# Kernel optimization log

Hardware: AMD Instinct MI355X
Metric: run time of the kernel (lower is better)

Reference implementation:

```python
import jax, jax.numpy as jnp
import numpy as np

H, W = 80, 80
LOWPASS = 0.3   # 3DGS low-pass filter added to 2D covariance diagonal
NEAR = 0.2      # near-plane cull depth


def quat_to_rot(q):
    # q: [N,4] (w,x,y,z) -> [N,3,3]
    w, x, y, z = q[..., 0], q[..., 1], q[..., 2], q[..., 3]
    return jnp.stack([
        jnp.stack([1 - 2 * (y * y + z * z), 2 * (x * y - w * z), 2 * (x * z + w * y)], -1),
        jnp.stack([2 * (x * y + w * z), 1 - 2 * (x * x + z * z), 2 * (y * z - w * x)], -1),
        jnp.stack([2 * (x * z - w * y), 2 * (y * z + w * x), 1 - 2 * (x * x + y * y)], -1),
    ], -2)


def setup_inputs() -> dict:
    key = jax.random.key(0)
    k1, k2 = jax.random.split(key)
    vsize = 1.25
    def mids(lo, hi, lim):
        g = np.arange(lo, hi + 1e-6, vsize)
        return ((g[:-1] + g[1:]) / 2.0)[:lim]
    xy = mids(-20.0, 20.0, 200)   # 32 midpoints
    zz = mids(-4.0, 4.0, 16)      # 6 midpoints
    X, Y, Z = np.meshgrid(xy, xy, zz, indexing='ij')
    pc_xyz = jnp.asarray(np.stack([X, Y, Z], -1).reshape(-1, 3), jnp.float32)  # [6144,3]
    N = pc_xyz.shape[0]
    B, NC, C = 1, 6, 32
    vox_features = jax.random.normal(k1, (B, N, C), jnp.float32)
    density = jax.random.normal(k2, (B, N), jnp.float32)
    scales = jnp.full((N, 1), float(np.log(vsize)), jnp.float32)
    rots = jnp.concatenate([jnp.ones((N, 1)), jnp.zeros((N, 3))], -1).astype(jnp.float32)
    # 6 surround cameras at origin, yaw = k*60deg; cam axes: x=right, y=up-ish, z=forward
    yaws = np.arange(NC) * (2 * np.pi / NC)
    f = np.stack([np.cos(yaws), np.sin(yaws), np.zeros(NC)], -1)
    r = np.stack([np.sin(yaws), -np.cos(yaws), np.zeros(NC)], -1)
    u = np.cross(f, r)
    Rw2c = np.stack([r, u, f], 1)  # rows are camera axes -> world2cam rotation [NC,3,3]
    cam_rot = jnp.asarray(Rw2c[None], jnp.float32)          # [B,NC,3,3]
    cam_trans = jnp.zeros((B, NC, 3), jnp.float32)          # [B,NC,3]
    cam_intr = jnp.asarray(np.tile(np.array([45.0, 45.0, W / 2.0, H / 2.0], np.float32), (B, NC, 1)))
    return dict(vox_features=vox_features, density=density, cam_rot=cam_rot,
                cam_trans=cam_trans, cam_intr=cam_intr, pc_xyz=pc_xyz,
                scales=scales, rots=rots)


def _render_one(Rcw, t, intr, pc_xyz, Mcov, opacity, feats):
    # Rcw [3,3], t [3], intr [4]; Mcov [N,3,3] = R*diag(s); opacity [N]; feats [N,C]
    fx, fy, cx, cy = intr[0], intr[1], intr[2], intr[3]
    cam = pc_xyz @ Rcw.T + t                    # [N,3] camera-frame means
    tz = jnp.maximum(cam[:, 2], 1e-6)
    valid = (cam[:, 2] > NEAR).astype(pc_xyz.dtype)
    u = fx * cam[:, 0] / tz + cx
    v = fy * cam[:, 1] / tz + cy
    z0 = jnp.zeros_like(tz)
    J = jnp.stack([jnp.stack([fx / tz, z0, -fx * cam[:, 0] / tz ** 2], -1),
                   jnp.stack([z0, fy / tz, -fy * cam[:, 1] / tz ** 2], -1)], -2)  # [N,2,3]
    A = jnp.einsum('nij,jk->nik', J, Rcw)       # J @ W  [N,2,3]
    Bm = jnp.einsum('nij,njk->nik', A, Mcov)    # [N,2,3]
    cov = jnp.einsum('nij,nkj->nik', Bm, Bm)    # 2D covariance [N,2,2]
    a = cov[:, 0, 0] + LOWPASS
    b = cov[:, 0, 1]
    c = cov[:, 1, 1] + LOWPASS
    det = a * c - b * b
    ia, ib, ic = c / det, -b / det, a / det
    # depth-sort (invalid gaussians pushed to the back)
    order = jnp.argsort(tz + (1.0 - valid) * 1e6)
    u, v, ia, ib, ic = u[order], v[order], ia[order], ib[order], ic[order]
    op_s, feat_s, valid_s = opacity[order], feats[order], valid[order]
    px = jnp.arange(W, dtype=pc_xyz.dtype)
    py = jnp.arange(H, dtype=pc_xyz.dtype)
    dx = px[None, None, :] - u[:, None, None]   # [N,1,W] -> broadcast [N,H,W]
    dy = py[None, :, None] - v[:, None, None]   # [N,H,1]
    power = (-0.5 * (ia[:, None, None] * dx * dx + ic[:, None, None] * dy * dy)
             - ib[:, None, None] * dx * dy)
    g = jnp.exp(jnp.minimum(power, 0.0))
    alpha = jnp.clip(op_s[:, None, None] * g, 0.0, 0.99) * valid_s[:, None, None]
    Tcum = jnp.cumprod(1.0 - alpha, axis=0)
    Texc = jnp.concatenate([jnp.ones((1, H, W), alpha.dtype), Tcum[:-1]], 0)  # exclusive transmittance
    return jnp.einsum('nhw,nc->chw', Texc * alpha, feat_s)


def reference(vox_features, density, cam_rot, cam_trans, cam_intr, pc_xyz, scales, rots):
    Bsz, N, C = vox_features.shape
    Rg = quat_to_rot(rots)                      # [N,3,3]
    s = jnp.exp(scales)                         # [N,1] isotropic scale
    Mcov = Rg * s[:, :, None]                   # R @ diag(s,s,s)
    outs = []
    for b in range(Bsz):
        op = jax.nn.softplus(density[b]).reshape(-1)        # opacity activation
        feats = vox_features[b].reshape(-1, C)
        def rone(args):
            R_, t_, K_ = args
            return _render_one(R_, t_, K_, pc_xyz, Mcov, op, feats)
        out_b = jax.lax.map(rone, (cam_rot[b], cam_trans[b], cam_intr[b]))  # [NC,C,H,W]
        outs.append(out_b)
    return jnp.stack(outs)                      # [B,NC,C,H,W]
```

## Files before the change

kernel.cpp:

```cpp
#include <hip/hip_runtime.h>

#define NEARV    0.2f
#define LOWPASSV 0.3f

constexpr int HH = 80, WW = 80;
constexpr int CFE = 32;
constexpr int NZ = 6;

constexpr int STHREADS = 1024;
constexpr int SWAVES = 16;
constexpr int SBINS = 512;
constexpr int NCELL = 1024;

typedef unsigned long long u64;
typedef unsigned int u32;

__global__ __launch_bounds__(1024) void sort_kernel(
    const float* __restrict__ pc_xyz, const float* __restrict__ cam_rot,
    const float* __restrict__ cam_trans, int N,
    int* __restrict__ counts, int* __restrict__ cellord)
{
  __shared__ u32 skey[NCELL];
  __shared__ u32 spay[NCELL];
  __shared__ u32 whist[SWAVES * SBINS];
  __shared__ u32 binstart[SBINS];
  __shared__ u32 wpart[8];
  __shared__ int scount;

  const int cam = blockIdx.x;
  const int tid = threadIdx.x;
  const int wv = tid >> 6, ln = tid & 63;
  const float* R = cam_rot + cam*9;
  const float R20 = R[6], R21 = R[7], R22 = R[8];
  const float t2  = cam_trans[cam*3+2];
  if (tid == 0) scount = 0;
  __syncthreads();

  const int i0 = tid * NZ;
  u32 kk = 0x07FFFFFFu;
  bool valid = false;
  if (i0 < N) {
    float c2 = R20*pc_xyz[i0*3+0] + R21*pc_xyz[i0*3+1] + R22*pc_xyz[i0*3+2] + t2;
    if (c2 > NEARV) {
      u32 b = __float_as_uint(c2) - 0x3E000000u;
      kk = b < 0x07FFFFFEu ? b : 0x07FFFFFEu;
      valid = true;
    }
  }
  skey[tid] = kk; spay[tid] = (u32)tid;
  u64 vb = __ballot(valid);
  if (ln == 0) atomicAdd(&scount, __popcll(vb));

  for (int pass = 0; pass < 3; ++pass) {
    const int sh = pass * 9;
    for (int i = tid; i < SWAVES*SBINS; i += STHREADS) whist[i] = 0;
    __syncthreads();

    const u32 k = skey[tid];
    const u32 p = spay[tid];
    const int d = (int)((k >> sh) & 511u);
    u64 m = ~0ull;
    #pragma unroll
    for (int b = 0; b < 9; ++b) {
      u64 bb = __ballot((d >> b) & 1);
      m &= ((d >> b) & 1) ? bb : ~bb;
    }
    const u32 lower = (u32)__popcll(m & ((1ull << ln) - 1ull));
    if (lower == 0) whist[(wv << 9) + d] = (u32)__popcll(m);
    __syncthreads();

    if (tid < SBINS) {
      u32 t[SWAVES];
      #pragma unroll
      for (int w = 0; w < SWAVES; ++w) t[w] = whist[(w << 9) + tid];
      u32 tot = 0;
      #pragma unroll
      for (int w = 0; w < SWAVES; ++w) { u32 x = t[w]; whist[(w << 9) + tid] = tot; tot += x; }
      binstart[tid] = tot;
    }
    __syncthreads();
    u32 v = 0, inc = 0;
    if (tid < SBINS) {
      v = binstart[tid]; inc = v;
      #pragma unroll
      for (int off = 1; off < 64; off <<= 1) {
        u32 t = __shfl_up(inc, off);
        if (ln >= off) inc += t;
      }
      if (ln == 63) wpart[tid >> 6] = inc;
    }
    __syncthreads();
    if (tid < SBINS) {
      u32 add = 0;
      for (int i = 0; i < (tid >> 6); ++i) add += wpart[i];
      binstart[tid] = add + inc - v;
    }
    __syncthreads();

    const u32 pos = binstart[d] + whist[(wv << 9) + d] + lower;
    skey[pos] = k; spay[pos] = p;
    __syncthreads();
  }

  const int vc = scount;
  if (tid < vc) cellord[(size_t)cam * NCELL + tid] = (int)spay[tid];
  if (tid == 0) counts[cam] = vc * NZ;
}

__global__ __launch_bounds__(64) void render_kernel(
    const float* __restrict__ vox, const float* __restrict__ density,
    const float* __restrict__ cam_rot, const float* __restrict__ cam_trans,
    const float* __restrict__ cam_intr, const float* __restrict__ pc_xyz,
    const float* __restrict__ scales,
    const int* __restrict__ counts, const int* __restrict__ cellord,
    float* __restrict__ out, int N, int NC)
{
  __shared__ float4 cA[64], cB[64];
  __shared__ int   cgi[64];
  __shared__ float4 sfeat[64 * 8];

  const int cam = blockIdx.y;
  const int tile = blockIdx.x;
  const int tx = tile % (WW/16), ty = tile / (WW/16);
  const int lane = threadIdx.x;
  const int lx = lane & 15, ly = lane >> 4;
  const int px = tx*16 + lx, py = ty*4 + ly;
  const float fpx = (float)px, fpy = (float)py;
  const float tx0 = (float)(tx*16), tx1 = tx0 + 15.f;
  const float ty0 = (float)(ty*4),  ty1 = ty0 + 3.f;
  const int count = counts[cam];
  const int b = cam / NC;
  const float* R = cam_rot + cam*9;
  const float* t = cam_trans + cam*3;
  const float* intr = cam_intr + cam*4;
  const float fx = intr[0], fy = intr[1], cx = intr[2], cy = intr[3];
  const int* coc = cellord + (size_t)cam * NCELL;

  float acc[CFE];
  #pragma unroll
  for (int i = 0; i < CFE; ++i) acc[i] = 0.f;
  float T = 1.0f;
  bool done = false;

  for (int k0 = 0; k0 < count && !done; k0 += 64) {
    const int ki = k0 + lane;
    const int kic = min(ki, count - 1);
    const int cell = kic / NZ;
    const int n = coc[cell] * NZ + (kic - cell * NZ);
    float p0 = pc_xyz[n*3+0], p1 = pc_xyz[n*3+1], p2 = pc_xyz[n*3+2];
    float c0 = R[0]*p0 + R[1]*p1 + R[2]*p2 + t[0];
    float c1 = R[3]*p0 + R[4]*p1 + R[5]*p2 + t[1];
    float c2 = R[6]*p0 + R[7]*p1 + R[8]*p2 + t[2];
    float tz = fmaxf(c2, 1e-6f);
    float itz = 1.0f / tz;
    float u = fx*c0*itz + cx;
    float v = fy*c1*itz + cy;
    float j00 = fx*itz,  j02 = -(fx*c0*itz)*itz;
    float j11 = fy*itz,  j12 = -(fy*c1*itz)*itz;
    float s = expf(scales[n]);
    float s2 = s*s;
    float cov00 = s2*(j00*j00 + j02*j02);
    float cov01 = s2*(j02*j12);
    float cov11 = s2*(j11*j11 + j12*j12);
    float a = cov00 + LOWPASSV, bb = cov01, cc = cov11 + LOWPASSV;
    float det = a*cc - bb*bb;
    float idet = 1.0f / det;
    float mid = 0.5f*(a + cc);
    float dd = sqrtf(fmaxf(mid*mid - det, 0.f));
    float r2 = (ki < count) ? 32.f * (mid + dd) : -1.f;
    float dens = density[(size_t)b*N + n];
    float op = fmaxf(dens, 0.f) + log1pf(expf(-fabsf(dens)));
    float ddx = fminf(fmaxf(u, tx0), tx1) - u;
    float ddy = fminf(fmaxf(v, ty0), ty1) - v;
    const bool hit = (ddx*ddx + ddy*ddy) <= r2;
    const u64 m = __ballot(hit);
    const int P = __popcll(m);
    if (P == 0) continue;
    __syncthreads();
    if (hit) {
      const int pos = (int)__popcll(m & ((1ull << lane) - 1ull));
      cA[pos] = make_float4(u, v, cc*idet, -bb*idet);
      cB[pos] = make_float4(a*idet, op, 0.f, 0.f);
      cgi[pos] = n;
    }
    __syncthreads();
    for (int s0 = 0; s0 < P; s0 += 8) {
      const int si = s0 + (lane >> 3);
      if (si < P) {
        const int gi = cgi[si];
        sfeat[si*8 + (lane & 7)] =
            ((const float4*)(vox + ((size_t)b*N + gi) * CFE))[lane & 7];
      }
    }
    __syncthreads();

    for (int j = 0; j < P && !done; j += 8) {
      float al[8];
      #pragma unroll
      for (int qq = 0; qq < 8; ++qq) {
        const int idx = j + qq;
        const float4 a0 = cA[idx & 63];
        const float4 a1 = cB[idx & 63];
        float dx = fpx - a0.x, dy = fpy - a0.y;
        float power = -0.5f*(a0.z*dx*dx + a1.x*dy*dy) - a0.w*dx*dy;
        float av = fminf(a1.y * __expf(fminf(power, 0.f)), 0.99f);
        av = (power > -16.f) ? av : 0.f;
        al[qq] = (idx < P) ? av : 0.f;
      }
      #pragma unroll
      for (int qq = 0; qq < 8; ++qq) {
        float w = T * al[qq];
        T -= w;
        if (__any(w > 1e-8f)) {
          const float4* fj = &sfeat[(j + qq) * 8];
          #pragma unroll
          for (int c8 = 0; c8 < CFE/4; ++c8) {
            float4 fv = fj[c8];
            acc[c8*4+0] += w*fv.x; acc[c8*4+1] += w*fv.y;
            acc[c8*4+2] += w*fv.z; acc[c8*4+3] += w*fv.w;
          }
        }
      }
      if (__all(T < 1e-4f)) done = true;
    }
  }
  float* ob = out + (((size_t)cam * CFE) * HH + py) * WW + px;
  #pragma unroll
  for (int c = 0; c < CFE; ++c) ob[(size_t)c * HH * WW] = acc[c];
}

extern "C" void kernel_launch(void* const* d_in, const int* in_sizes, int n_in,
                              void* d_out, int out_size, void* d_ws, size_t ws_size,
                              hipStream_t stream) {
  const float* vox       = (const float*)d_in[0];
  const float* density   = (const float*)d_in[1];
  const float* cam_rot   = (const float*)d_in[2];
  const float* cam_trans = (const float*)d_in[3];
  const float* cam_intr  = (const float*)d_in[4];
  const float* pc_xyz    = (const float*)d_in[5];
  const float* scales    = (const float*)d_in[6];
  float* out = (float*)d_out;

  const int N    = in_sizes[5] / 3;
  const int NCAM = in_sizes[4] / 4;
  const int B    = in_sizes[1] / N;
  const int NC   = NCAM / B;

  unsigned char* ws = (unsigned char*)d_ws;
  int* countsPtr = (int*)ws;
  int* cellord = (int*)(ws + 256);

  sort_kernel<<<dim3(NCAM), STHREADS, 0, stream>>>(
      pc_xyz, cam_rot, cam_trans, N, countsPtr, cellord);
  render_kernel<<<dim3((WW/16)*(HH/4), NCAM), 64, 0, stream>>>(
      vox, density, cam_rot, cam_trans, cam_intr, pc_xyz, scales,
      countsPtr, cellord, out, N, NC);
}
```

Measured before the change: 84.06 us.

## Precompute per-camera splat headers with screen culling in sort kernel, prefetch in render

The sort kernel now projects each depth-sorted Gaussian once per camera, computing 2D conic, opacity, radius and index, and culls splats whose footprint misses the image. It compacts the survivors into per-camera header arrays in workspace. The render kernel no longer recomputes the projection for every tile. Instead it loads precomputed headers with a one-batch register prefetch and double-buffers feature loads in 8-splat chunks through a smaller shared buffer. This removes redundant projection math across 100 tiles per camera, at the cost of a serial compaction loop in a single block per camera and extra barriers per chunk.

```diff
diff --git a/kernel.cpp b/kernel.cpp
--- a/kernel.cpp
+++ b/kernel.cpp
@@ -11,36 +11,41 @@
 constexpr int SWAVES = 16;
 constexpr int SBINS = 512;
 constexpr int NCELL = 1024;
+constexpr int HMAX = NCELL * NZ;
 
 typedef unsigned long long u64;
 typedef unsigned int u32;
 
 __global__ __launch_bounds__(1024) void sort_kernel(
     const float* __restrict__ pc_xyz, const float* __restrict__ cam_rot,
-    const float* __restrict__ cam_trans, int N,
-    int* __restrict__ counts, int* __restrict__ cellord)
+    const float* __restrict__ cam_trans, const float* __restrict__ cam_intr,
+    const float* __restrict__ density, const float* __restrict__ scales,
+    int N, int NC,
+    int* __restrict__ counts, float4* __restrict__ hdrA,
+    float4* __restrict__ hdrB)
 {
   __shared__ u32 skey[NCELL];
   __shared__ u32 spay[NCELL];
   __shared__ u32 whist[SWAVES * SBINS];
   __shared__ u32 binstart[SBINS];
   __shared__ u32 wpart[8];
+  __shared__ u32 wsum[SWAVES];
   __shared__ int scount;
+  __shared__ int obase;
 
   const int cam = blockIdx.x;
   const int tid = threadIdx.x;
   const int wv = tid >> 6, ln = tid & 63;
   const float* R = cam_rot + cam*9;
-  const float R20 = R[6], R21 = R[7], R22 = R[8];
-  const float t2  = cam_trans[cam*3+2];
-  if (tid == 0) scount = 0;
+  const float* t = cam_trans + cam*3;
+  if (tid == 0) { scount = 0; obase = 0; }
   __syncthreads();
 
   const int i0 = tid * NZ;
   u32 kk = 0x07FFFFFFu;
   bool valid = false;
   if (i0 < N) {
-    float c2 = R20*pc_xyz[i0*3+0] + R21*pc_xyz[i0*3+1] + R22*pc_xyz[i0*3+2] + t2;
+    float c2 = R[6]*pc_xyz[i0*3+0] + R[7]*pc_xyz[i0*3+1] + R[8]*pc_xyz[i0*3+2] + t[2];
     if (c2 > NEARV) {
       u32 b = __float_as_uint(c2) - 0x3E000000u;
       kk = b < 0x07FFFFFEu ? b : 0x07FFFFFEu;
@@ -70,12 +75,12 @@
     __syncthreads();
 
     if (tid < SBINS) {
-      u32 t[SWAVES];
+      u32 tt[SWAVES];
       #pragma unroll
-      for (int w = 0; w < SWAVES; ++w) t[w] = whist[(w << 9) + tid];
+      for (int w = 0; w < SWAVES; ++w) tt[w] = whist[(w << 9) + tid];
       u32 tot = 0;
       #pragma unroll
-      for (int w = 0; w < SWAVES; ++w) { u32 x = t[w]; whist[(w << 9) + tid] = tot; tot += x; }
+      for (int w = 0; w < SWAVES; ++w) { u32 x = tt[w]; whist[(w << 9) + tid] = tot; tot += x; }
       binstart[tid] = tot;
     }
     __syncthreads();
@@ -84,8 +89,8 @@
       v = binstart[tid]; inc = v;
       #pragma unroll
       for (int off = 1; off < 64; off <<= 1) {
-        u32 t = __shfl_up(inc, off);
-        if (ln >= off) inc += t;
+        u32 tq = __shfl_up(inc, off);
+        if (ln >= off) inc += tq;
       }
       if (ln == 63) wpart[tid >> 6] = inc;
     }
@@ -103,21 +108,82 @@
   }
 
   const int vc = scount;
-  if (tid < vc) cellord[(size_t)cam * NCELL + tid] = (int)spay[tid];
-  if (tid == 0) counts[cam] = vc * NZ;
+  const int total = vc * NZ;
+  const float* intr = cam_intr + cam*4;
+  const float fx = intr[0], fy = intr[1], cx = intr[2], cy = intr[3];
+  const float R0=R[0],R1=R[1],R2=R[2],R3=R[3],R4=R[4],R5=R[5],R6=R[6],R7=R[7],R8=R[8];
+  const float t0=t[0],t1=t[1],t2=t[2];
+  const int b = cam / NC;
+  float4* hA = hdrA + (size_t)cam * HMAX;
+  float4* hB = hdrB + (size_t)cam * HMAX;
+
+  for (int k0 = 0; k0 < total; k0 += STHREADS) {
+    const int kq = k0 + tid;
+    bool keep = false;
+    float4 va = make_float4(0.f,0.f,0.f,0.f);
+    float4 vbh = make_float4(0.f,0.f,0.f,0.f);
+    if (kq < total) {
+      const int cellp = kq / NZ;
+      const int n = (int)spay[cellp] * NZ + (kq - cellp * NZ);
+      const float p0 = pc_xyz[n*3+0], p1 = pc_xyz[n*3+1], p2 = pc_xyz[n*3+2];
+      const float c0 = R0*p0 + R1*p1 + R2*p2 + t0;
+      const float c1 = R3*p0 + R4*p1 + R5*p2 + t1;
+      const float c2 = R6*p0 + R7*p1 + R8*p2 + t2;
+      const float tz = fmaxf(c2, 1e-6f);
+      const float itz = 1.0f / tz;
+      const float u = fx*c0*itz + cx;
+      const float v = fy*c1*itz + cy;
+      const float j00 = fx*itz, j02 = -(fx*c0*itz)*itz;
+      const float j11 = fy*itz, j12 = -(fy*c1*itz)*itz;
+      const float s = expf(scales[n]);
+      const float s2 = s*s;
+      const float cov00 = s2*(j00*j00 + j02*j02);
+      const float cov01 = s2*(j02*j12);
+      const float cov11 = s2*(j11*j11 + j12*j12);
+      const float a = cov00 + LOWPASSV, bb = cov01, cc = cov11 + LOWPASSV;
+      const float det = a*cc - bb*bb;
+      const float idet = 1.0f / det;
+      const float mid = 0.5f*(a + cc);
+      const float dd = sqrtf(fmaxf(mid*mid - det, 0.f));
+      const float r2 = 32.f * (mid + dd);
+      const float dens = density[(size_t)b*N + n];
+      const float op = fmaxf(dens, 0.f) + log1pf(expf(-fabsf(dens)));
+      const float sx = fminf(fmaxf(u, 0.f), (float)(WW-1)) - u;
+      const float sy = fminf(fmaxf(v, 0.f), (float)(HH-1)) - v;
+      keep = (sx*sx + sy*sy) <= r2;
+      va  = make_float4(u, v, cc*idet, -bb*idet);
+      vbh = make_float4(a*idet, op, r2, __int_as_float(n));
+    }
+    const u64 bal = __ballot(keep);
+    if (ln == 0) wsum[wv] = (u32)__popcll(bal);
+    __syncthreads();
+    if (keep) {
+      u32 off = 0;
+      for (int w = 0; w < wv; ++w) off += wsum[w];
+      const int pos = obase + (int)(off + (u32)__popcll(bal & ((1ull << ln) - 1ull)));
+      hA[pos] = va; hB[pos] = vbh;
+    }
+    __syncthreads();
+    if (tid == 0) {
+      u32 tot = 0;
+      #pragma unroll
+      for (int w = 0; w < SWAVES; ++w) tot += wsum[w];
+      obase += (int)tot;
+    }
+    __syncthreads();
+  }
+  if (tid == 0) counts[cam] = obase;
 }
 
 __global__ __launch_bounds__(64) void render_kernel(
-    const float* __restrict__ vox, const float* __restrict__ density,
-    const float* __restrict__ cam_rot, const float* __restrict__ cam_trans,
-    const float* __restrict__ cam_intr, const float* __restrict__ pc_xyz,
-    const float* __restrict__ scales,
-    const int* __restrict__ counts, const int* __restrict__ cellord,
+    const float* __restrict__ vox,
+    const float4* __restrict__ hdrA, const float4* __restrict__ hdrB,
+    const int* __restrict__ counts,
     float* __restrict__ out, int N, int NC)
 {
   __shared__ float4 cA[64], cB[64];
   __shared__ int   cgi[64];
-  __shared__ float4 sfeat[64 * 8];
+  __shared__ float4 sfeat[64];
 
   const int cam = blockIdx.y;
   const int tile = blockIdx.x;
@@ -130,11 +196,9 @@
   const float ty0 = (float)(ty*4),  ty1 = ty0 + 3.f;
   const int count = counts[cam];
   const int b = cam / NC;
-  const float* R = cam_rot + cam*9;
-  const float* t = cam_trans + cam*3;
-  const float* intr = cam_intr + cam*4;
-  const float fx = intr[0], fy = intr[1], cx = intr[2], cy = intr[3];
-  const int* coc = cellord + (size_t)cam * NCELL;
+  const float4* hA = hdrA + (size_t)cam * HMAX;
+  const float4* hB = hdrB + (size_t)cam * HMAX;
+  const float4* voxb = (const float4*)vox + (size_t)b * N * (CFE/4);
 
   float acc[CFE];
   #pragma unroll
@@ -142,86 +206,72 @@
   float T = 1.0f;
   bool done = false;
 
-  for (int k0 = 0; k0 < count && !done; k0 += 64) {
-    const int ki = k0 + lane;
-    const int kic = min(ki, count - 1);
-    const int cell = kic / NZ;
-    const int n = coc[cell] * NZ + (kic - cell * NZ);
-    float p0 = pc_xyz[n*3+0], p1 = pc_xyz[n*3+1], p2 = pc_xyz[n*3+2];
-    float c0 = R[0]*p0 + R[1]*p1 + R[2]*p2 + t[0];
-    float c1 = R[3]*p0 + R[4]*p1 + R[5]*p2 + t[1];
-    float c2 = R[6]*p0 + R[7]*p1 + R[8]*p2 + t[2];
-    float tz = fmaxf(c2, 1e-6f);
-    float itz = 1.0f / tz;
-    float u = fx*c0*itz + cx;
-    float v = fy*c1*itz + cy;
-    float j00 = fx*itz,  j02 = -(fx*c0*itz)*itz;
-    float j11 = fy*itz,  j12 = -(fy*c1*itz)*itz;
-    float s = expf(scales[n]);
-    float s2 = s*s;
-    float cov00 = s2*(j00*j00 + j02*j02);
-    float cov01 = s2*(j02*j12);
-    float cov11 = s2*(j11*j11 + j12*j12);
-    float a = cov00 + LOWPASSV, bb = cov01, cc = cov11 + LOWPASSV;
-    float det = a*cc - bb*bb;
-    float idet = 1.0f / det;
-    float mid = 0.5f*(a + cc);
-    float dd = sqrtf(fmaxf(mid*mid - det, 0.f));
-    float r2 = (ki < count) ? 32.f * (mid + dd) : -1.f;
-    float dens = density[(size_t)b*N + n];
-    float op = fmaxf(dens, 0.f) + log1pf(expf(-fabsf(dens)));
-    float ddx = fminf(fmaxf(u, tx0), tx1) - u;
-    float ddy = fminf(fmaxf(v, ty0), ty1) - v;
-    const bool hit = (ddx*ddx + ddy*ddy) <= r2;
-    const u64 m = __ballot(hit);
-    const int P = __popcll(m);
-    if (P == 0) continue;
-    __syncthreads();
-    if (hit) {
-      const int pos = (int)__popcll(m & ((1ull << lane) - 1ull));
-      cA[pos] = make_float4(u, v, cc*idet, -bb*idet);
-      cB[pos] = make_float4(a*idet, op, 0.f, 0.f);
-      cgi[pos] = n;
-    }
-    __syncthreads();
-    for (int s0 = 0; s0 < P; s0 += 8) {
-      const int si = s0 + (lane >> 3);
-      if (si < P) {
-        const int gi = cgi[si];
-        sfeat[si*8 + (lane & 7)] =
-            ((const float4*)(vox + ((size_t)b*N + gi) * CFE))[lane & 7];
+  if (count > 0) {
+    const int kcf = min(lane, count - 1);
+    float4 na = hA[kcf], nb = hB[kcf];
+
+    for (int k0 = 0; k0 < count && !done; k0 += 64) {
+      const float4 a0 = na, b0 = nb;
+      if (k0 + 64 < count) {
+        const int kn = min(k0 + 64 + lane, count - 1);
+        na = hA[kn]; nb = hB[kn];
       }
-    }
-    __syncthreads();
-
-    for (int j = 0; j < P && !done; j += 8) {
-      float al[8];
-      #pragma unroll
-      for (int qq = 0; qq < 8; ++qq) {
-        const int idx = j + qq;
-        const float4 a0 = cA[idx & 63];
-        const float4 a1 = cB[idx & 63];
-        float dx = fpx - a0.x, dy = fpy - a0.y;
-        float power = -0.5f*(a0.z*dx*dx + a1.x*dy*dy) - a0.w*dx*dy;
-        float av = fminf(a1.y * __expf(fminf(power, 0.f)), 0.99f);
-        av = (power > -16.f) ? av : 0.f;
-        al[qq] = (idx < P) ? av : 0.f;
+      const int ki = k0 + lane;
+      const float ddx = fminf(fmaxf(a0.x, tx0), tx1) - a0.x;
+      const float ddy = fminf(fmaxf(a0.y, ty0), ty1) - a0.y;
+      const bool hit = (ki < count) && (ddx*ddx + ddy*ddy <= b0.z);
+      const u64 m = __ballot(hit);
+      const int P = __popcll(m);
+      if (P == 0) continue;
+      __syncthreads();
+      if (hit) {
+        const int pos = (int)__popcll(m & ((1ull << lane) - 1ull));
+        cA[pos] = a0;
+        cB[pos] = b0;
+        cgi[pos] = __float_as_int(b0.w);
       }
-      #pragma unroll
-      for (int qq = 0; qq < 8; ++qq) {
-        float w = T * al[qq];
-        T -= w;
-        if (__any(w > 1e-8f)) {
-          const float4* fj = &sfeat[(j + qq) * 8];
-          #pragma unroll
-          for (int c8 = 0; c8 < CFE/4; ++c8) {
-            float4 fv = fj[c8];
-            acc[c8*4+0] += w*fv.x; acc[c8*4+1] += w*fv.y;
-            acc[c8*4+2] += w*fv.z; acc[c8*4+3] += w*fv.w;
+      __syncthreads();
+
+      const int sl = lane >> 3, sc = lane & 7;
+      float4 pf = voxb[(size_t)cgi[min(sl, P - 1)] * (CFE/4) + sc];
+
+      for (int j = 0; j < P; j += 8) {
+        sfeat[lane] = pf;
+        if (j + 8 < P) {
+          const int si = min(j + 8 + sl, P - 1);
+          pf = voxb[(size_t)cgi[si] * (CFE/4) + sc];
+        }
+        __syncthreads();
+
+        float al[8];
+        #pragma unroll
+        for (int qq = 0; qq < 8; ++qq) {
+          const int idx = j + qq;
+          const float4 a1 = cA[idx & 63];
+          const float4 a2 = cB[idx & 63];
+          const float dx = fpx - a1.x, dy = fpy - a1.y;
+          const float power = -0.5f*(a1.z*dx*dx + a2.x*dy*dy) - a1.w*dx*dy;
+          float av = fminf(a2.y * __expf(fminf(power, 0.f)), 0.99f);
+          av = (power > -16.f) ? av : 0.f;
+          al[qq] = (idx < P) ? av : 0.f;
+        }
+        #pragma unroll
+        for (int qq = 0; qq < 8; ++qq) {
+          const float w = T * al[qq];
+          T -= w;
+          if (__any(w > 1e-8f)) {
+            const float4* fj = &sfeat[qq * 8];
+            #pragma unroll
+            for (int c8 = 0; c8 < CFE/4; ++c8) {
+              const float4 fv = fj[c8];
+              acc[c8*4+0] += w*fv.x; acc[c8*4+1] += w*fv.y;
+              acc[c8*4+2] += w*fv.z; acc[c8*4+3] += w*fv.w;
+            }
           }
         }
+        if (__all(T < 1e-4f)) { done = true; break; }
+        __syncthreads();
       }
-      if (__all(T < 1e-4f)) done = true;
     }
   }
   float* ob = out + (((size_t)cam * CFE) * HH + py) * WW + px;
@@ -248,11 +298,12 @@
 
   unsigned char* ws = (unsigned char*)d_ws;
   int* countsPtr = (int*)ws;
-  int* cellord = (int*)(ws + 256);
+  float4* hdrA = (float4*)(ws + 256);
+  float4* hdrB = (float4*)(ws + 256 + (size_t)NCAM * HMAX * sizeof(float4));
 
   sort_kernel<<<dim3(NCAM), STHREADS, 0, stream>>>(
-      pc_xyz, cam_rot, cam_trans, N, countsPtr, cellord);
+      pc_xyz, cam_rot, cam_trans, cam_intr, density, scales, N, NC,
+      countsPtr, hdrA, hdrB);
   render_kernel<<<dim3((WW/16)*(HH/4), NCAM), 64, 0, stream>>>(
-      vox, density, cam_rot, cam_trans, cam_intr, pc_xyz, scales,
-      countsPtr, cellord, out, N, NC);
+      vox, hdrA, hdrB, countsPtr, out, N, NC);
 }
```

Result: slower. 89.21 us (+6.1%).
